# Optimization experiments

Measured on AMD Instinct MI355X. Metric: run time of the kernel, lower is better.

## Reference

```python
import jax, jax.numpy as jnp
import numpy as np

B, NQ, NK, D, DV = 16, 2048, 2048, 128, 128


def setup_inputs() -> dict:
    key = jax.random.key(0)
    kq, kk, kv, kl = jax.random.split(key, 4)
    return {
        "queries": jax.random.normal(kq, (B, NQ, D), dtype=jnp.float32),
        "keys": jax.random.normal(kk, (B, NK, D), dtype=jnp.float32),
        "values": jax.random.normal(kv, (B, NK, DV), dtype=jnp.float32),
        "valid_lens": jax.random.randint(kl, (B,), 1, NK + 1, dtype=jnp.int32),
    }


def reference(queries, keys, values, valid_lens):
    d = queries.shape[-1]
    # scores: [B, NQ, NK]
    scores = jnp.einsum("bqd,bkd->bqk", queries, keys) / jnp.sqrt(jnp.float32(d))
    # mask positions >= valid_len with -1e6 (matches sequence_mask semantics)
    key_pos = jnp.arange(scores.shape[-1], dtype=jnp.int32)  # [NK]
    mask = key_pos[None, None, :] < valid_lens[:, None, None]  # [B,1,NK] -> broadcast over queries
    scores = jnp.where(mask, scores, jnp.float32(-1000000.0))
    attn = jax.nn.softmax(scores, axis=-1)
    # dropout p=0.0 -> identity
    return jnp.einsum("bqk,bkv->bqv", attn, values)
```

## Files before the change

### kernel.cpp

```cpp
#include <hip/hip_runtime.h>


#define B_   16
#define NQ_  2048
#define NK_  2048
#define D_   128
#define DV_  128
#define NTASK_ 512

typedef unsigned short ushort;
typedef __attribute__((ext_vector_type(4))) float          f32x4;
typedef __attribute__((ext_vector_type(8))) __bf16         bf16x8;
typedef __attribute__((ext_vector_type(8))) unsigned short ushort8v;
typedef __attribute__((ext_vector_type(4))) unsigned int   uint4v;

#ifdef __has_builtin
#if __has_builtin(__builtin_amdgcn_cvt_pk_bf16_f32)
#define HAVE_CVT_PK_BF16 1
#endif
#endif

__device__ __forceinline__ ushort f2bf(float f) {
    unsigned u = __builtin_bit_cast(unsigned, f);
    return (ushort)((u + 0x8000u) >> 16);
}
__device__ __forceinline__ unsigned f2bf2(float a, float b) {
#ifdef HAVE_CVT_PK_BF16
    auto t = __builtin_amdgcn_cvt_pk_bf16_f32(a, b);
    return __builtin_bit_cast(unsigned, t);
#else
    return (unsigned)f2bf(a) | ((unsigned)f2bf(b) << 16);
#endif
}
__device__ __forceinline__ float bfpair_sum(unsigned u) {
    float lo = __builtin_bit_cast(float, u << 16);
    float hi = __builtin_bit_cast(float, u & 0xffff0000u);
    return lo + hi;
}
__device__ __forceinline__ void gl_lds16(const ushort* g, ushort* l) {
    __builtin_amdgcn_global_load_lds(
        (const __attribute__((address_space(1))) void*)g,
        (__attribute__((address_space(3))) void*)l, 16, 0, 0);
}

#define VL_STRIDE 132
__global__ __launch_bounds__(256) void convert_kv(
    const float* __restrict__ K, const float* __restrict__ V,
    const int* __restrict__ vlen, ushort* __restrict__ Kb, ushort* __restrict__ Vtb)
{
    __shared__ ushort Vl[64 * VL_STRIDE];
    const int id = blockIdx.x;
    const int b  = id & 15, kt = id >> 4;
    if (kt >= ((vlen[b] + 63) >> 6)) return;
    const int tid = threadIdx.x;
    const float* gK = K + ((size_t)b * NK_ + kt * 64) * D_;
    const float* gV = V + ((size_t)b * NK_ + kt * 64) * DV_;
    ushort* tK = Kb  + ((size_t)b * 32 + kt) * 8192;
    ushort* tV = Vtb + ((size_t)b * 32 + kt) * 8192;

    #pragma unroll
    for (int i = 0; i < 4; ++i) {
        int u = i * 256 + tid;
        int key = u >> 4, d8 = u & 15;
        const float* p = gK + key * D_ + d8 * 8;
        f32x4 a0 = *(const f32x4*)p;
        f32x4 a1 = *(const f32x4*)(p + 4);
        uint4v w;
        w[0] = f2bf2(a0[0], a0[1]); w[1] = f2bf2(a0[2], a0[3]);
        w[2] = f2bf2(a1[0], a1[1]); w[3] = f2bf2(a1[2], a1[3]);
        *(uint4v*)&tK[key * 128 + ((d8 ^ (key & 7)) << 3)] = w;
    }

    #pragma unroll
    for (int i = 0; i < 4; ++i) {
        int u = i * 256 + tid;
        int key = u >> 4, d8 = u & 15;
        const float* p = gV + key * DV_ + d8 * 8;
        f32x4 a0 = *(const f32x4*)p;
        f32x4 a1 = *(const f32x4*)(p + 4);
        uint4v w;
        w[0] = f2bf2(a0[0], a0[1]); w[1] = f2bf2(a0[2], a0[3]);
        w[2] = f2bf2(a1[0], a1[1]); w[3] = f2bf2(a1[2], a1[3]);
        *(uint4v*)&Vl[key * VL_STRIDE + d8 * 8] = w;
    }
    __syncthreads();

    #pragma unroll
    for (int i = 0; i < 4; ++i) {
        int u  = i * 256 + tid;
        int c  = u & 7, dv = u >> 3;
        int kg = c ^ (dv & 7);
        ushort v[8];
        #pragma unroll
        for (int j = 0; j < 8; ++j) v[j] = Vl[(kg * 8 + j) * VL_STRIDE + dv];
        uint4v w;
        w[0] = (unsigned)v[0] | ((unsigned)v[1] << 16);
        w[1] = (unsigned)v[2] | ((unsigned)v[3] << 16);
        w[2] = (unsigned)v[4] | ((unsigned)v[5] << 16);
        w[3] = (unsigned)v[6] | ((unsigned)v[7] << 16);
        *(uint4v*)&tV[dv * 64 + c * 8] = w;
    }
}

__global__ __launch_bounds__(512, 4) void attn_fwd(
    const float* __restrict__ Q, const int* __restrict__ vlen,
    const ushort* __restrict__ Kb, const ushort* __restrict__ Vtb,
    float* __restrict__ Out)
{
    __shared__ ushort KVbuf[2][16384];
    __shared__ float  lsh[2][64];
    __shared__ int    ssch[16];
    float* Osh = (float*)&KVbuf[0][0];

    const int tid  = threadIdx.x;
    const int w    = tid >> 6;
    const int wq   = w >> 2;
    const int wk   = (w >> 1) & 1;
    const int wd   = w & 1;
    const int L    = tid & 63;
    const int col  = L & 15;
    const int quad = L >> 4;

    if (tid < 16) {
        int my = vlen[tid];
        int rank = 0;
        for (int o = 0; o < 16; ++o) {
            int vo = vlen[o];
            if (vo > my || (vo == my && o < tid)) ++rank;
        }
        ssch[rank] = tid;
    }
    __syncthreads();

    const int e     = blockIdx.x;
    const int p_    = (e & 255) >> 5;
    const int b     = (e >> 8) ? ssch[15 - p_] : ssch[p_];
    const int qbase = (e & 31) * 64;
    const int vl    = vlen[b];
    const int ntiles = (vl + 63) >> 6;

    const float qscale = 0.12751743f;
    bf16x8 qf[2][4];
    #pragma unroll
    for (int q16 = 0; q16 < 2; ++q16) {
        const int qrow = qbase + wq * 32 + q16 * 16 + col;
        const float* gQ = Q + ((size_t)b * NQ_ + qrow) * D_;
        #pragma unroll
        for (int c = 0; c < 4; ++c) {
            const float* pp = gQ + c * 32 + quad * 8;
            f32x4 a0 = *(const f32x4*)pp;
            f32x4 a1 = *(const f32x4*)(pp + 4);
            uint4v us;
            us[0] = f2bf2(a0[0] * qscale, a0[1] * qscale);
            us[1] = f2bf2(a0[2] * qscale, a0[3] * qscale);
            us[2] = f2bf2(a1[0] * qscale, a1[1] * qscale);
            us[3] = f2bf2(a1[2] * qscale, a1[3] * qscale);
            qf[q16][c] = __builtin_bit_cast(bf16x8, us);
        }
    }

    f32x4 o[2][4];
    #pragma unroll
    for (int q16 = 0; q16 < 2; ++q16)
        #pragma unroll
        for (int d = 0; d < 4; ++d) o[q16][d] = (f32x4){0.f, 0.f, 0.f, 0.f};
    float l_run[2] = {0.f, 0.f};

    const ushort* tKb = Kb  + (size_t)b * 32 * 8192;
    const ushort* tVb = Vtb + (size_t)b * 32 * 8192;

    #define ISSUE_DMA(KT, BUF)                                               \
        do {                                                                 \
            const ushort* gk = tKb + (size_t)(KT) * 8192;                    \
            const ushort* gv = tVb + (size_t)(KT) * 8192;                    \
            _Pragma("unroll")                                                \
            for (int i = 0; i < 2; ++i) {                                    \
                int off = (i * 512 + tid) * 8;                               \
                gl_lds16(gk + off, &KVbuf[BUF][off]);                        \
                gl_lds16(gv + off, &KVbuf[BUF][8192 + off]);                 \
            }                                                                \
        } while (0)

    ISSUE_DMA(0, 0);

    const int swz = col & 7;

    for (int kt = 0; kt < ntiles; ++kt) {
        const int buf = kt & 1;
        __syncthreads();
        if (kt + 1 < ntiles) ISSUE_DMA(kt + 1, buf ^ 1);

        const ushort* Kt = &KVbuf[buf][0];
        const ushort* Vt = &KVbuf[buf][8192];

        f32x4 s[2][2];
        #pragma unroll
        for (int q16 = 0; q16 < 2; ++q16)
            #pragma unroll
            for (int kc = 0; kc < 2; ++kc) s[q16][kc] = (f32x4){0.f,0.f,0.f,0.f};
        __builtin_amdgcn_s_setprio(1);
        #pragma unroll
        for (int kc = 0; kc < 2; ++kc) {
            const int kbase = (wk * 32 + kc * 16 + col) * 128;
            #pragma unroll
            for (int c = 0; c < 4; ++c) {
                bf16x8 kb = __builtin_bit_cast(bf16x8, *(const ushort8v*)
                    &Kt[kbase + (((c * 4 + quad) ^ swz) << 3)]);
                s[0][kc] = __builtin_amdgcn_mfma_f32_16x16x32_bf16(kb, qf[0][c], s[0][kc], 0, 0, 0);
                s[1][kc] = __builtin_amdgcn_mfma_f32_16x16x32_bf16(kb, qf[1][c], s[1][kc], 0, 0, 0);
            }
        }
        __builtin_amdgcn_s_setprio(0);

        const int rem = vl - kt * 64 - wk * 32;
        if (rem < 32) {
            #pragma unroll
            for (int rr = 0; rr < 4; ++rr) {
                if (quad * 4 + rr >= rem) {
                    s[0][0][rr] = -1e30f; s[1][0][rr] = -1e30f;
                }
                if (16 + quad * 4 + rr >= rem) {
                    s[0][1][rr] = -1e30f; s[1][1][rr] = -1e30f;
                }
            }
        }

        bf16x8 pa[2];
        #pragma unroll
        for (int q16 = 0; q16 < 2; ++q16) {
            unsigned wA = f2bf2(exp2f(s[q16][0][0]), exp2f(s[q16][0][1]));
            unsigned wB = f2bf2(exp2f(s[q16][0][2]), exp2f(s[q16][0][3]));
            unsigned wC = f2bf2(exp2f(s[q16][1][0]), exp2f(s[q16][1][1]));
            unsigned wD = f2bf2(exp2f(s[q16][1][2]), exp2f(s[q16][1][3]));
            l_run[q16] += bfpair_sum(wA) + bfpair_sum(wB) + bfpair_sum(wC) + bfpair_sum(wD);
            asm("v_permlane32_swap_b32 %0, %1" : "+v"(wA), "+v"(wC));
            asm("v_permlane32_swap_b32 %0, %1" : "+v"(wB), "+v"(wD));
            asm("v_permlane16_swap_b32 %0, %1" : "+v"(wA), "+v"(wC));
            asm("v_permlane16_swap_b32 %0, %1" : "+v"(wB), "+v"(wD));
            uint4v pw;
            pw[0] = wA; pw[1] = wB; pw[2] = wC; pw[3] = wD;
            pa[q16] = __builtin_bit_cast(bf16x8, pw);
        }

        __builtin_amdgcn_s_setprio(1);
        #pragma unroll
        for (int dvc = 0; dvc < 4; ++dvc) {
            const int dv = (wd * 4 + dvc) * 16 + col;
            bf16x8 vb = __builtin_bit_cast(bf16x8, *(const ushort8v*)
                &Vt[dv * 64 + (((wk * 4 + quad) ^ swz) << 3)]);
            o[0][dvc] = __builtin_amdgcn_mfma_f32_16x16x32_bf16(pa[0], vb, o[0][dvc], 0, 0, 0);
            o[1][dvc] = __builtin_amdgcn_mfma_f32_16x16x32_bf16(pa[1], vb, o[1][dvc], 0, 0, 0);
        }
        __builtin_amdgcn_s_setprio(0);
    }
    #undef ISSUE_DMA

    #pragma unroll
    for (int q16 = 0; q16 < 2; ++q16) {
        l_run[q16] += __shfl_xor(l_run[q16], 16, 64);
        l_run[q16] += __shfl_xor(l_run[q16], 32, 64);
    }

    __syncthreads();

    if (wd == 0 && L < 16) {
        lsh[wk][wq * 32 + L]      = l_run[0];
        lsh[wk][wq * 32 + 16 + L] = l_run[1];
    }
    #pragma unroll
    for (int q16 = 0; q16 < 2; ++q16)
        #pragma unroll
        for (int dvc = 0; dvc < 4; ++dvc)
            #pragma unroll
            for (int rr = 0; rr < 4; ++rr)
                Osh[wk * 8192 + (wq * 32 + q16 * 16 + quad * 4 + rr) * 128
                    + (wd * 4 + dvc) * 16 + col] = o[q16][dvc][rr];
    __syncthreads();

    float* gO = Out + ((size_t)b * NQ_ + qbase) * DV_;
    #pragma unroll
    for (int i = 0; i < 4; ++i) {
        int idx = i * 512 + tid;
        int row = idx >> 5;
        int dq  = idx & 31;
        f32x4 a0 = *(const f32x4*)&Osh[row * 128 + dq * 4];
        f32x4 a1 = *(const f32x4*)&Osh[8192 + row * 128 + dq * 4];
        float linv = 1.0f / (lsh[0][row] + lsh[1][row]);
        *(f32x4*)&gO[(size_t)row * DV_ + dq * 4] = (a0 + a1) * linv;
    }
}

extern "C" void kernel_launch(void* const* d_in, const int* in_sizes, int n_in,
                              void* d_out, int out_size, void* d_ws, size_t ws_size,
                              hipStream_t stream) {
    const float* Q  = (const float*)d_in[0];
    const float* K  = (const float*)d_in[1];
    const float* V  = (const float*)d_in[2];
    const int*   vl = (const int*)d_in[3];
    float* out = (float*)d_out;

    char* ws = (char*)d_ws;
    ushort* Kbuf = (ushort*)(ws + 4096);
    ushort* Vbuf = Kbuf + (size_t)B_ * 32 * 8192;

    convert_kv<<<dim3(512, 1, 1), dim3(256, 1, 1), 0, stream>>>(K, V, vl, Kbuf, Vbuf);
    attn_fwd<<<dim3(NTASK_, 1, 1), dim3(512, 1, 1), 0, stream>>>(
        Q, vl, Kbuf, Vbuf, out);
}
```

Before: 145.6 us.

## Split each key tile four ways across waves and use 16x16x16 MFMA for PV

Each wave now owns 16 keys of the 64-key tile and all 128 value columns, replacing the old 2-key by 2-dv wave split. Because the score fragment layout now matches the 16x16x16 bf16 MFMA operand layout directly, the permlane swaps that repacked probabilities for the 16x16x32 instruction are dropped. In exchange, the accumulator registers per wave double, each wave reads V at a narrower 8-byte granularity, and the epilogue needs an extra barrier and a read-modify-write pass to reduce four partial outputs and four row sums.

Measured after the change: 146.8 us. No clear change (+0.8%).

```diff
diff --git a/kernel.cpp b/kernel.cpp
--- a/kernel.cpp
+++ b/kernel.cpp
@@ -12,11 +12,17 @@
 typedef __attribute__((ext_vector_type(4))) float          f32x4;
 typedef __attribute__((ext_vector_type(8))) __bf16         bf16x8;
 typedef __attribute__((ext_vector_type(8))) unsigned short ushort8v;
+typedef __attribute__((ext_vector_type(4))) unsigned short ushort4v;
+typedef __attribute__((ext_vector_type(4))) short          short4v;
 typedef __attribute__((ext_vector_type(4))) unsigned int   uint4v;
+typedef __attribute__((ext_vector_type(2))) unsigned int   uint2v;
 
 #ifdef __has_builtin
 #if __has_builtin(__builtin_amdgcn_cvt_pk_bf16_f32)
 #define HAVE_CVT_PK_BF16 1
+#endif
+#if __has_builtin(__builtin_amdgcn_mfma_f32_16x16x16bf16_1k)
+#define HAVE_MFMA16_1K 1
 #endif
 #endif
 
@@ -41,6 +47,14 @@
     __builtin_amdgcn_global_load_lds(
         (const __attribute__((address_space(1))) void*)g,
         (__attribute__((address_space(3))) void*)l, 16, 0, 0);
+}
+__device__ __forceinline__ f32x4 mfma16(short4v a, short4v b, f32x4 c) {
+#ifdef HAVE_MFMA16_1K
+    return __builtin_amdgcn_mfma_f32_16x16x16bf16_1k(a, b, c, 0, 0, 0);
+#else
+    asm("v_mfma_f32_16x16x16_bf16 %0, %1, %2, %0" : "+v"(c) : "v"(a), "v"(b));
+    return c;
+#endif
 }
 
 #define VL_STRIDE 132
@@ -108,15 +122,14 @@
     float* __restrict__ Out)
 {
     __shared__ ushort KVbuf[2][16384];
-    __shared__ float  lsh[2][64];
+    __shared__ float  lsh[4][64];
     __shared__ int    ssch[16];
     float* Osh = (float*)&KVbuf[0][0];
 
     const int tid  = threadIdx.x;
     const int w    = tid >> 6;
     const int wq   = w >> 2;
-    const int wk   = (w >> 1) & 1;
-    const int wd   = w & 1;
+    const int wk   = w & 3;
     const int L    = tid & 63;
     const int col  = L & 15;
     const int quad = L >> 4;
@@ -159,11 +172,11 @@
         }
     }
 
-    f32x4 o[2][4];
+    f32x4 o[2][8];
     #pragma unroll
     for (int q16 = 0; q16 < 2; ++q16)
         #pragma unroll
-        for (int d = 0; d < 4; ++d) o[q16][d] = (f32x4){0.f, 0.f, 0.f, 0.f};
+        for (int d = 0; d < 8; ++d) o[q16][d] = (f32x4){0.f, 0.f, 0.f, 0.f};
     float l_run[2] = {0.f, 0.f};
 
     const ushort* tKb = Kb  + (size_t)b * 32 * 8192;
@@ -184,6 +197,8 @@
     ISSUE_DMA(0, 0);
 
     const int swz = col & 7;
+    const int vkg  = wk * 2 + (quad >> 1);
+    const int vsub = (quad & 1) * 4;
 
     for (int kt = 0; kt < ntiles; ++kt) {
         const int buf = kt & 1;
@@ -193,63 +208,47 @@
         const ushort* Kt = &KVbuf[buf][0];
         const ushort* Vt = &KVbuf[buf][8192];
 
-        f32x4 s[2][2];
-        #pragma unroll
-        for (int q16 = 0; q16 < 2; ++q16)
-            #pragma unroll
-            for (int kc = 0; kc < 2; ++kc) s[q16][kc] = (f32x4){0.f,0.f,0.f,0.f};
+        f32x4 s[2];
+        s[0] = (f32x4){0.f,0.f,0.f,0.f};
+        s[1] = (f32x4){0.f,0.f,0.f,0.f};
         __builtin_amdgcn_s_setprio(1);
-        #pragma unroll
-        for (int kc = 0; kc < 2; ++kc) {
-            const int kbase = (wk * 32 + kc * 16 + col) * 128;
+        {
+            const int kbase = (wk * 16 + col) * 128;
             #pragma unroll
             for (int c = 0; c < 4; ++c) {
                 bf16x8 kb = __builtin_bit_cast(bf16x8, *(const ushort8v*)
                     &Kt[kbase + (((c * 4 + quad) ^ swz) << 3)]);
-                s[0][kc] = __builtin_amdgcn_mfma_f32_16x16x32_bf16(kb, qf[0][c], s[0][kc], 0, 0, 0);
-                s[1][kc] = __builtin_amdgcn_mfma_f32_16x16x32_bf16(kb, qf[1][c], s[1][kc], 0, 0, 0);
+                s[0] = __builtin_amdgcn_mfma_f32_16x16x32_bf16(kb, qf[0][c], s[0], 0, 0, 0);
+                s[1] = __builtin_amdgcn_mfma_f32_16x16x32_bf16(kb, qf[1][c], s[1], 0, 0, 0);
             }
         }
         __builtin_amdgcn_s_setprio(0);
 
-        const int rem = vl - kt * 64 - wk * 32;
-        if (rem < 32) {
+        const int rem = vl - kt * 64 - wk * 16;
+        if (rem < 16) {
             #pragma unroll
-            for (int rr = 0; rr < 4; ++rr) {
-                if (quad * 4 + rr >= rem) {
-                    s[0][0][rr] = -1e30f; s[1][0][rr] = -1e30f;
-                }
-                if (16 + quad * 4 + rr >= rem) {
-                    s[0][1][rr] = -1e30f; s[1][1][rr] = -1e30f;
-                }
-            }
-        }
-
-        bf16x8 pa[2];
+            for (int rr = 0; rr < 4; ++rr)
+                if (quad * 4 + rr >= rem) { s[0][rr] = -1e30f; s[1][rr] = -1e30f; }
+        }
+
+        short4v pa[2];
         #pragma unroll
         for (int q16 = 0; q16 < 2; ++q16) {
-            unsigned wA = f2bf2(exp2f(s[q16][0][0]), exp2f(s[q16][0][1]));
-            unsigned wB = f2bf2(exp2f(s[q16][0][2]), exp2f(s[q16][0][3]));
-            unsigned wC = f2bf2(exp2f(s[q16][1][0]), exp2f(s[q16][1][1]));
-            unsigned wD = f2bf2(exp2f(s[q16][1][2]), exp2f(s[q16][1][3]));
-            l_run[q16] += bfpair_sum(wA) + bfpair_sum(wB) + bfpair_sum(wC) + bfpair_sum(wD);
-            asm("v_permlane32_swap_b32 %0, %1" : "+v"(wA), "+v"(wC));
-            asm("v_permlane32_swap_b32 %0, %1" : "+v"(wB), "+v"(wD));
-            asm("v_permlane16_swap_b32 %0, %1" : "+v"(wA), "+v"(wC));
-            asm("v_permlane16_swap_b32 %0, %1" : "+v"(wB), "+v"(wD));
-            uint4v pw;
-            pw[0] = wA; pw[1] = wB; pw[2] = wC; pw[3] = wD;
-            pa[q16] = __builtin_bit_cast(bf16x8, pw);
+            unsigned w0 = f2bf2(exp2f(s[q16][0]), exp2f(s[q16][1]));
+            unsigned w1 = f2bf2(exp2f(s[q16][2]), exp2f(s[q16][3]));
+            l_run[q16] += bfpair_sum(w0) + bfpair_sum(w1);
+            uint2v t; t[0] = w0; t[1] = w1;
+            pa[q16] = __builtin_bit_cast(short4v, t);
         }
 
         __builtin_amdgcn_s_setprio(1);
         #pragma unroll
-        for (int dvc = 0; dvc < 4; ++dvc) {
-            const int dv = (wd * 4 + dvc) * 16 + col;
-            bf16x8 vb = __builtin_bit_cast(bf16x8, *(const ushort8v*)
-                &Vt[dv * 64 + (((wk * 4 + quad) ^ swz) << 3)]);
-            o[0][dvc] = __builtin_amdgcn_mfma_f32_16x16x32_bf16(pa[0], vb, o[0][dvc], 0, 0, 0);
-            o[1][dvc] = __builtin_amdgcn_mfma_f32_16x16x32_bf16(pa[1], vb, o[1][dvc], 0, 0, 0);
+        for (int dvc = 0; dvc < 8; ++dvc) {
+            const int dv = dvc * 16 + col;
+            short4v vb = __builtin_bit_cast(short4v, *(const ushort4v*)
+                &Vt[dv * 64 + ((vkg ^ (dv & 7)) << 3) + vsub]);
+            o[0][dvc] = mfma16(pa[0], vb, o[0][dvc]);
+            o[1][dvc] = mfma16(pa[1], vb, o[1][dvc]);
         }
         __builtin_amdgcn_s_setprio(0);
     }
@@ -263,18 +262,31 @@
 
     __syncthreads();
 
-    if (wd == 0 && L < 16) {
+    if (L < 16) {
         lsh[wk][wq * 32 + L]      = l_run[0];
         lsh[wk][wq * 32 + 16 + L] = l_run[1];
     }
-    #pragma unroll
-    for (int q16 = 0; q16 < 2; ++q16)
-        #pragma unroll
-        for (int dvc = 0; dvc < 4; ++dvc)
+    if (wk < 2) {
+        #pragma unroll
+        for (int q16 = 0; q16 < 2; ++q16)
             #pragma unroll
-            for (int rr = 0; rr < 4; ++rr)
-                Osh[wk * 8192 + (wq * 32 + q16 * 16 + quad * 4 + rr) * 128
-                    + (wd * 4 + dvc) * 16 + col] = o[q16][dvc][rr];
+            for (int dvc = 0; dvc < 8; ++dvc)
+                #pragma unroll
+                for (int rr = 0; rr < 4; ++rr)
+                    Osh[wk * 8192 + (wq * 32 + q16 * 16 + quad * 4 + rr) * 128
+                        + dvc * 16 + col] = o[q16][dvc][rr];
+    }
+    __syncthreads();
+    if (wk >= 2) {
+        #pragma unroll
+        for (int q16 = 0; q16 < 2; ++q16)
+            #pragma unroll
+            for (int dvc = 0; dvc < 8; ++dvc)
+                #pragma unroll
+                for (int rr = 0; rr < 4; ++rr)
+                    Osh[(wk - 2) * 8192 + (wq * 32 + q16 * 16 + quad * 4 + rr) * 128
+                        + dvc * 16 + col] += o[q16][dvc][rr];
+    }
     __syncthreads();
 
     float* gO = Out + ((size_t)b * NQ_ + qbase) * DV_;
@@ -285,7 +297,7 @@
         int dq  = idx & 31;
         f32x4 a0 = *(const f32x4*)&Osh[row * 128 + dq * 4];
         f32x4 a1 = *(const f32x4*)&Osh[8192 + row * 128 + dq * 4];
-        float linv = 1.0f / (lsh[0][row] + lsh[1][row]);
+        float linv = 1.0f / (lsh[0][row] + lsh[1][row] + lsh[2][row] + lsh[3][row]);
         *(f32x4*)&gO[(size_t)row * DV_ + dq * 4] = (a0 + a1) * linv;
     }
 }
```
